# Kernel optimization log

Hardware: AMD Instinct MI355X
Metric: run time of the kernel (lower is better)

Reference implementation:

```python
import jax, jax.numpy as jnp
import numpy as np

B, L, K, NRBF = 2, 2048, 32, 16
NODE_F, EDGE_F = 128, 128
MAX_REL = 32  # af2 relpos -> 2*32+1 = 65 bins
NODE_IN, EDGE_IN = 21 + 6 + 8, 65 + 25 * NRBF + 1 + 2


def _ln(x, g, b, eps=1e-5):
    mu = jnp.mean(x, -1, keepdims=True)
    var = jnp.var(x, -1, keepdims=True)
    return (x - mu) / jnp.sqrt(var + eps) * g + b


def _normalize(t):
    return jnp.nan_to_num(t / jnp.linalg.norm(t, axis=-1, keepdims=True))


def _dihedral(p0, p1, p2, p3):
    u0, u1, u2 = p2 - p1, p0 - p1, p3 - p2
    n1 = _normalize(jnp.cross(u0, u1))
    n2 = _normalize(jnp.cross(u0, u2))
    sgn = jnp.sign(jnp.sum(jnp.cross(u1, u2) * u0, -1))
    return jnp.nan_to_num(sgn * jnp.arccos(jnp.sum(n1 * n2, -1)))


def setup_inputs() -> dict:
    key = jax.random.key(0)
    ks = jax.random.split(key, 9)
    return {
        "X": jax.random.normal(ks[0], (B, L, 4, 3), jnp.float32) * 5.0,
        "S": jax.random.randint(ks[1], (B, L), 0, 21),
        "BB_D_sincos": jax.random.normal(ks[2], (B, L, 3, 2), jnp.float32),
        "SC_D_sincos": jax.random.normal(ks[3], (B, L, 4, 2), jnp.float32),
        "chain_indices": jax.random.randint(ks[4], (B, L), 0, 2),
        "mask": jnp.ones((B, L), jnp.float32),
        "W_node": jax.random.normal(ks[5], (NODE_IN, NODE_F), jnp.float32) * 0.05,
        "b_node": jnp.zeros((NODE_F,), jnp.float32),
        "g_node": jnp.ones((NODE_F,), jnp.float32),
        "beta_node": jnp.zeros((NODE_F,), jnp.float32),
        "W_edge": jax.random.normal(ks[6], (EDGE_IN, EDGE_F), jnp.float32) * 0.05,
        "b_edge": jnp.zeros((EDGE_F,), jnp.float32),
        "g_edge": jnp.ones((EDGE_F,), jnp.float32),
        "beta_edge": jnp.zeros((EDGE_F,), jnp.float32),
    }


def reference(X, S, BB_D_sincos, SC_D_sincos, chain_indices, mask,
              W_node, b_node, g_node, beta_node,
              W_edge, b_edge, g_edge, beta_edge):
    Bn, Ln = X.shape[:2]
    N, Ca, C, O = X[:, :, 0], X[:, :, 1], X[:, :, 2], X[:, :, 3]
    # ---- masked pairwise Ca distances + kNN topk (smallest) ----
    m2 = mask[:, None, :] * mask[:, :, None]                      # [B,L,L]
    dX = Ca[:, :, None, :] - Ca[:, None, :, :]
    D = m2 * jnp.sqrt(jnp.sum(dX * dX, -1) + 1e-6)
    D_adj = D + 2.0 * (1.0 - m2) * jnp.max(D, -1, keepdims=True)
    _, E_idx = jax.lax.top_k(-D_adj, K)                           # [B,L,K]
    bidx = jnp.arange(Bn)[:, None, None]
    # ---- af2 relative-position one-hot (residue_index=None path) ----
    offset = E_idx - jnp.arange(Ln)[None, :, None]
    E_pos = jax.nn.one_hot(jnp.clip(offset + MAX_REL, 0, 2 * MAX_REL),
                           2 * MAX_REL + 1, dtype=jnp.float32)    # [B,L,K,65]
    # ---- impute CB, 5x5 atomic-distance RBFs at neighbors only ----
    bv, cv = Ca - N, C - Ca
    Cb = -0.58273431 * jnp.cross(bv, cv) + 0.56802827 * bv - 0.54067466 * cv + Ca
    X5 = jnp.stack((N, Ca, C, O, Cb), axis=-2)                    # [B,L,5,3]
    X5_nb = X5[bidx, E_idx]                                       # [B,L,K,5,3]
    dA = X5[:, :, None, :, None, :] - X5_nb[:, :, :, None, :, :]  # [B,L,K,5i,5j,3]
    Dn = jnp.sqrt(jnp.sum(dA * dA, -1) + 1e-6)                    # [B,L,K,5,5]
    mu = jnp.linspace(0.0, 20.0, NRBF)
    sigma = 20.0 / NRBF
    RBF_all = jnp.exp(-(((Dn[..., None] - mu) / sigma) ** 2))
    RBF_all = RBF_all.reshape(Bn, Ln, K, 25 * NRBF)               # i-major, j, rbf order
    # ---- edge type: same-chain indicator + 1 ----
    ch_nb = chain_indices[bidx, E_idx]
    E_type = ((ch_nb == chain_indices[:, :, None]).astype(jnp.float32) + 1.0)[..., None]
    # ---- pairwise dihedrals, evaluated only at neighbors ----
    N_nb, Ca_nb, C_nb = N[bidx, E_idx], Ca[bidx, E_idx], C[bidx, E_idx]
    ir_phi = _dihedral(C[:, :, None, :], N_nb, Ca_nb, C_nb)
    ir_psi = _dihedral(N[:, :, None, :], Ca[:, :, None, :], C[:, :, None, :], N_nb)
    dihed = jnp.stack((ir_phi, ir_psi), -1)                       # [B,L,K,2]
    # ---- fuse + embed ----
    E = jnp.concatenate((E_pos, RBF_all, E_type, dihed), -1)      # [B,L,K,468]
    V = jnp.concatenate((jax.nn.one_hot(S, 21, dtype=jnp.float32),
                         BB_D_sincos.reshape(Bn, Ln, -1),
                         SC_D_sincos.reshape(Bn, Ln, -1)), -1)    # [B,L,35]
    h_V = _ln(V @ W_node + b_node, g_node, beta_node)
    h_E = _ln(E @ W_edge + b_edge, g_edge, beta_edge)
    return (h_V, h_E, E_idx, X)
```

## Files before the change

kernel.cpp:

```cpp
#include <hip/hip_runtime.h>
#include <math.h>

#define NB 2
#define NL 2048
#define NK 32
#define NODE_F 128
#define EDGE_F 128

#define OFF_HV   0
#define OFF_HE   (NB*NL*NODE_F)
#define OFF_EIDX (OFF_HE + NB*NL*NK*EDGE_F)
#define OFF_X    (OFF_EIDX + NB*NL*NK)

#define ACH 8
#define BCH 8
#define SAW 264
#define NCH 16

typedef __attribute__((ext_vector_type(8))) short v8s;
typedef __attribute__((ext_vector_type(4))) float v4f;

__device__ __forceinline__ short f2bf(float f) {
    unsigned u = __float_as_uint(f);
    unsigned r = u + 0x7fffu + ((u >> 16) & 1u);
    return (short)(r >> 16);
}

#if __has_builtin(__builtin_amdgcn_exp2f)
#define EXP2F(x) __builtin_amdgcn_exp2f(x)
#else
#define EXP2F(x) __expf((x) * 0.6931471805599453f)
#endif

__device__ __forceinline__ unsigned bfpack(float f0, float f1) {
    unsigned u0 = __float_as_uint(f0), u1 = __float_as_uint(f1);
#if __has_builtin(__builtin_amdgcn_perm)
    return __builtin_amdgcn_perm(u1, u0, 0x07060302u);
#else
    return (u1 & 0xFFFF0000u) | (u0 >> 16);
#endif
}

template<int CTRL>
__device__ __forceinline__ float dpp_add_f32(float x) {
    int p = __builtin_amdgcn_update_dpp(0, __float_as_int(x), CTRL, 0xF, 0xF, true);
    return x + __int_as_float(p);
}
template<int CTRL>
__device__ __forceinline__ float dpp_max_f32(float x) {
    int p = __builtin_amdgcn_update_dpp(0, __float_as_int(x), CTRL, 0xF, 0xF, true);
    return fmaxf(x, __int_as_float(p));
}
__device__ __forceinline__ float dpp_row_sum16(float x) {
    x = dpp_add_f32<0x111>(x);
    x = dpp_add_f32<0x112>(x);
    x = dpp_add_f32<0x114>(x);
    x = dpp_add_f32<0x118>(x);
    return x;
}
__device__ __forceinline__ float dpp_wave_sum(float x) {
    x = dpp_row_sum16(x);
    x = dpp_add_f32<0x142>(x);
    x = dpp_add_f32<0x143>(x);
    return __int_as_float(__builtin_amdgcn_readlane(__float_as_int(x), 63));
}
__device__ __forceinline__ float dpp_wave_max_nn(float x) {
    x = dpp_max_f32<0x111>(x);
    x = dpp_max_f32<0x112>(x);
    x = dpp_max_f32<0x114>(x);
    x = dpp_max_f32<0x118>(x);
    x = dpp_max_f32<0x142>(x);
    x = dpp_max_f32<0x143>(x);
    return __int_as_float(__builtin_amdgcn_readlane(__float_as_int(x), 63));
}

template<int J>
__device__ __forceinline__ unsigned long long lane_xor64(unsigned long long x) {
    if constexpr (J == 32) {
        return __shfl_xor(x, 32, 64);
    } else {
        unsigned lo = (unsigned)x, hi = (unsigned)(x >> 32);
        if constexpr (J == 1 || J == 2) {
            constexpr int ctrl = (J == 1) ? 0xB1 : 0x4E;
            lo = (unsigned)__builtin_amdgcn_update_dpp((int)lo, (int)lo, ctrl, 0xF, 0xF, false);
            hi = (unsigned)__builtin_amdgcn_update_dpp((int)hi, (int)hi, ctrl, 0xF, 0xF, false);
        } else {
            constexpr int off = (J << 10) | 0x1F;
            lo = (unsigned)__builtin_amdgcn_ds_swizzle((int)lo, off);
            hi = (unsigned)__builtin_amdgcn_ds_swizzle((int)hi, off);
        }
        return (((unsigned long long)hi) << 32) | lo;
    }
}

__device__ __forceinline__ void cross3(const float a[3], const float b[3], float c[3]) {
    c[0] = a[1]*b[2] - a[2]*b[1];
    c[1] = a[2]*b[0] - a[0]*b[2];
    c[2] = a[0]*b[1] - a[1]*b[0];
}
__device__ __forceinline__ float dot3(const float a[3], const float b[3]) {
    return a[0]*b[0] + a[1]*b[1] + a[2]*b[2];
}
__device__ float dihedral_f(const float p0[3], const float p1[3],
                            const float p2[3], const float p3[3]) {
    float u0[3], u1[3], u2[3];
    for (int d = 0; d < 3; d++) {
        u0[d] = p2[d] - p1[d];
        u1[d] = p0[d] - p1[d];
        u2[d] = p3[d] - p2[d];
    }
    float n1[3], n2[3], c12[3];
    cross3(u0, u1, n1);
    cross3(u0, u2, n2);
    cross3(u1, u2, c12);
    float l1 = sqrtf(dot3(n1, n1));
    float l2 = sqrtf(dot3(n2, n2));
    float cosang = dot3(n1, n2) / (l1 * l2);
    float s = dot3(c12, u0);
    float sgn = (s > 0.f) ? 1.f : ((s < 0.f) ? -1.f : 0.f);
    float r = sgn * acosf(cosang);
    return isnan(r) ? 0.f : r;
}

__global__ __launch_bounds__(256) void fused_pre_kernel(const float* __restrict__ X,
                                                        const float* __restrict__ mask,
                                                        const int* __restrict__ S,
                                                        const float* __restrict__ BB,
                                                        const float* __restrict__ SC,
                                                        const float* __restrict__ Wn,
                                                        const float* __restrict__ bn,
                                                        const float* __restrict__ gn,
                                                        const float* __restrict__ betan,
                                                        const float* __restrict__ We,
                                                        const float* __restrict__ be,
                                                        float* __restrict__ X5,
                                                        short* __restrict__ WTf,
                                                        int* __restrict__ EidxW,
                                                        float* __restrict__ out) {
    __shared__ float sCa[NL * 3];
    __shared__ unsigned long long sSel[4][64];
    int blk = blockIdx.x;
    int tid = threadIdx.x;

    if (blk >= 1024) {
        if (blk < 1040) {
            int row = (blk - 1024) * 256 + tid;
            float v[12];
#pragma unroll
            for (int t = 0; t < 12; t++) v[t] = X[row * 12 + t];
#pragma unroll
            for (int t = 0; t < 12; t++) out[OFF_X + row * 12 + t] = v[t];
            float bv[3], cv[3], cr[3];
            for (int d = 0; d < 3; d++) { bv[d] = v[3+d] - v[d]; cv[d] = v[6+d] - v[3+d]; }
            cross3(bv, cv, cr);
            float* x5 = X5 + row * 15;
#pragma unroll
            for (int t = 0; t < 12; t++) x5[t] = v[t];
            for (int d = 0; d < 3; d++)
                x5[12 + d] = -0.58273431f * cr[d] + 0.56802827f * bv[d] - 0.54067466f * cv[d] + v[3+d];
        } else {
            int t = (blk - 1040) * 256 + tid;
            if (t >= NCH * 8 * 64) return;
            int lane = t & 63;
            int nt = (t >> 6) & 7;
            int ch = t >> 9;
            int n = nt * 16 + (lane & 15);
            int kbase = ch * 32 + (lane >> 4) * 8;
            short* dst = WTf + (size_t)t * 8;
#pragma unroll
            for (int j = 0; j < 8; j++) {
                int k = kbase + j;
                float f;
                if (k < 403) f = We[(65 + k) * 128 + n];
                else if (k == 403) f = be[n];
                else if (k <= 468) f = We[(k - 404) * 128 + n];
                else f = 0.f;
                dst[j] = f2bf(f);
            }
        }
        return;
    }

    int w = tid >> 6, l = tid & 63;
    int row = blk * 4 + w;
    int b = row / NL;
    int base = b * NL;

    for (int idx = tid; idx < NL; idx += 256) {
        const float* xp = X + (size_t)(base + idx) * 12 + 3;
        sCa[idx * 3 + 0] = xp[0];
        sCa[idx * 3 + 1] = xp[1];
        sCa[idx * 3 + 2] = xp[2];
    }

    {
        int f0 = l, f1 = 64 + l;
        int s = S[row];
        float a0 = bn[f0] + Wn[s * NODE_F + f0];
        float a1 = bn[f1] + Wn[s * NODE_F + f1];
#pragma unroll
        for (int t = 0; t < 6; t++) {
            float x = BB[row * 6 + t];
            a0 += x * Wn[(21 + t) * NODE_F + f0];
            a1 += x * Wn[(21 + t) * NODE_F + f1];
        }
#pragma unroll
        for (int t = 0; t < 8; t++) {
            float x = SC[row * 8 + t];
            a0 += x * Wn[(27 + t) * NODE_F + f0];
            a1 += x * Wn[(27 + t) * NODE_F + f1];
        }
        float tot = dpp_wave_sum(a0 + a1);
        float mean = tot * (1.0f / 128.0f);
        float d0 = a0 - mean, d1 = a1 - mean;
        float qt = dpp_wave_sum(d0 * d0 + d1 * d1);
        float rstd = 1.0f / sqrtf(qt * (1.0f / 128.0f) + 1e-5f);
        out[OFF_HV + row * NODE_F + f0] = d0 * rstd * gn[f0] + betan[f0];
        out[OFF_HV + row * NODE_F + f1] = d1 * rstd * gn[f1] + betan[f1];
    }
    __syncthreads();

    const float* mrow = mask + base;
    int lrow = row - base;
    float cx = sCa[lrow * 3 + 0], cy = sCa[lrow * 3 + 1], cz = sCa[lrow * 3 + 2];
    float mi = mrow[lrow];

    float K[32];
    float lmax = 0.0f;
#pragma unroll
    for (int t = 0; t < 32; t++) {
        int j = t * 64 + l;
        float dx = __fsub_rn(cx, sCa[j * 3 + 0]);
        float dy = __fsub_rn(cy, sCa[j * 3 + 1]);
        float dz = __fsub_rn(cz, sCa[j * 3 + 2]);
        float ss = __fadd_rn(__fadd_rn(__fadd_rn(__fmul_rn(dx, dx), __fmul_rn(dy, dy)),
                                       __fmul_rn(dz, dz)), 1e-6f);
        float d = __fmul_rn(__fmul_rn(mi, mrow[j]), __fsqrt_rn(ss));
        K[t] = d;
        lmax = fmaxf(lmax, d);
    }
    lmax = dpp_wave_max_nn(lmax);
#pragma unroll
    for (int t = 0; t < 32; t++) {
        int j = t * 64 + l;
        float m2 = __fmul_rn(mi, mrow[j]);
        K[t] = __fadd_rn(K[t], __fmul_rn(__fmul_rn(2.0f, __fsub_rn(1.0f, m2)), lmax));
    }

    unsigned lo_ = 0u, hi_ = 0x7f7fffffu, tau = 0x7f7fffffu;
#pragma unroll 1
    for (int it = 0; it < 31; it++) {
        unsigned mid = (lo_ + hi_) >> 1;
        float tf = __uint_as_float(mid);
        int c = 0;
#pragma unroll
        for (int t = 0; t < 32; t++) c += __popcll(__ballot(K[t] <= tf));
        if (c >= 32) {
            tau = mid;
            if (c <= 64) break;
            hi_ = mid - 1;
        } else {
            lo_ = mid + 1;
        }
    }
    float tauf = __uint_as_float(tau);

    sSel[w][l] = ~0ull;
    int cbase = 0;
#pragma unroll
    for (int t = 0; t < 32; t++) {
        bool q = (K[t] <= tauf);
        unsigned long long m = __ballot(q);
        int pos = cbase + __popcll(m & ((1ull << l) - 1ull));
        if (q && pos < 64)
            sSel[w][pos] = (((unsigned long long)__float_as_uint(K[t])) << 32)
                           | (unsigned)(t * 64 + l);
        cbase += __popcll(m);
    }

    unsigned long long key = sSel[w][l];
#define BSTAGE(K_, J_) {                                                       \
    unsigned long long o_ = lane_xor64<J_>(key);                               \
    bool keepMin = (((l & (K_)) == 0) == ((l & (J_)) == 0));                   \
    unsigned long long mn_ = key < o_ ? key : o_;                              \
    key = keepMin ? mn_ : (key ^ o_ ^ mn_);                                    \
}
    BSTAGE(2, 1)
    BSTAGE(4, 2)  BSTAGE(4, 1)
    BSTAGE(8, 4)  BSTAGE(8, 2)  BSTAGE(8, 1)
    BSTAGE(16, 8) BSTAGE(16, 4) BSTAGE(16, 2) BSTAGE(16, 1)
    BSTAGE(32, 16) BSTAGE(32, 8) BSTAGE(32, 4) BSTAGE(32, 2) BSTAGE(32, 1)
    BSTAGE(64, 32) BSTAGE(64, 16) BSTAGE(64, 8) BSTAGE(64, 4) BSTAGE(64, 2) BSTAGE(64, 1)

    if (l < NK) {
        int selj = (int)(unsigned)key;
        EidxW[row * NK + l] = selj;
        out[OFF_EIDX + row * NK + l] = (float)selj;
    }
}

__global__ __launch_bounds__(256, 4) void edge11_kernel(const float* __restrict__ X5,
                                                        const int* __restrict__ Eidx,
                                                        const int* __restrict__ chain,
                                                        const float* __restrict__ ge,
                                                        const float* __restrict__ betae,
                                                        const short* __restrict__ WTf,
                                                        float* __restrict__ out) {
    __shared__ short sA[64 * SAW];
    __shared__ float sXj[64][17];
    __shared__ float sXi[2][15];
    __shared__ int   sJ[64];
    __shared__ int   sPos[64];
    __shared__ float sEt[64], sPhi[64], sPsi[64];

    int tid = threadIdx.x;
    int e0 = blockIdx.x * 64;
    int b = e0 / (NL * NK);
    int i0 = (e0 / NK) % NL;
    int lane = tid & 63, w = tid >> 6;

    if (tid < 64) sJ[tid] = Eidx[e0 + tid];
    if (tid < 30) sXi[tid / 15][tid % 15] = X5[(b * NL + i0 + tid / 15) * 15 + (tid % 15)];
    __syncthreads();

    for (int t = tid; t < 64 * 15; t += 256) {
        int e = t / 15, c2 = t % 15;
        sXj[e][c2] = X5[(b * NL + sJ[e]) * 15 + c2];
    }
    if (tid < 64) {
        int e = tid;
        int i = i0 + (e >> 5);
        int j = sJ[e];
        int off = j - i + 32;
        off = off < 0 ? 0 : (off > 64 ? 64 : off);
        sPos[e] = off;
        sEt[e] = (chain[b * NL + j] == chain[b * NL + i]) ? 2.0f : 1.0f;
    }
    __syncthreads();

    if (tid < 128) {
        int e = tid & 63;
        const float* xi = sXi[e >> 5];
        const float* xj = sXj[e];
        if (tid < 64) sPhi[e] = dihedral_f(&xi[6], &xj[0], &xj[3], &xj[6]);
        else          sPsi[e] = dihedral_f(&xi[0], &xi[3], &xi[6], &xj[0]);
    }

    const float Ac  = -0.92332482616893658f;
    const float K1c = 2.46219953645049755f;
    const float Rc  = EXP2F(-1.64146635763366503f);
    const float R2c = Rc * Rc;
    int eg_ = w * 16 + (lane & 15);
    int q_ = lane >> 4;
    const float* xiG = sXi[eg_ >> 5];
    const float* xjG = sXj[eg_];
    short* rowp = sA + eg_ * SAW;
    int posG = sPos[eg_];

#define SPECV(k) ((k) == 400 ? sEt[eg_] : (k) == 401 ? sPhi[eg_] : (k) == 402 ? sPsi[eg_] : \
                  (k) == 403 ? 1.0f : (((k) - 404 == posG) ? 1.0f : 0.0f))

#define GEN_A(hh)                                                              \
    {                                                                          \
        _Pragma("unroll")                                                      \
        for (int t = 0; t < 4; t++) {                                          \
            int pl = q_ + t * 4;                         \
            int p  = (hh) * 16 + pl;                          \
            union { unsigned u[8]; v8s v[2]; } au;                             \
            if ((hh) == 1 && p >= 25) {                                        \
                _Pragma("unroll")                                              \
                for (int jp = 0; jp < 8; jp++) {                               \
                    int k0 = p * 16 + 2 * jp;                                  \
                    au.u[jp] = bfpack(SPECV(k0), SPECV(k0 + 1));               \
                }                                                              \
            } else {                                                           \
                int a = p / 5, cc = p - a * 5;                                 \
                float dx = xiG[a*3+0] - xjG[cc*3+0];                           \
                float dy = xiG[a*3+1] - xjG[cc*3+1];                           \
                float dz = xiG[a*3+2] - xjG[cc*3+2];                           \
                float d = sqrtf(dx*dx + dy*dy + dz*dz + 1e-6f);                \
                float ee = fminf(d, 40.f);                                     \
                float r0 = EXP2F(Ac * ee * ee);                                \
                float g  = EXP2F(K1c * ee) * Rc;                               \
                float r1  = r0  * g; g *= R2c;                                 \
                float r2  = r1  * g; g *= R2c;                                 \
                float r3  = r2  * g; g *= R2c;                                 \
                float r4  = r3  * g; g *= R2c;                                 \
                float r5  = r4  * g; g *= R2c;                                 \
                float r6  = r5  * g; g *= R2c;                                 \
                float r7  = r6  * g; g *= R2c;                                 \
                float r8  = r7  * g; g *= R2c;                                 \
                float r9  = r8  * g; g *= R2c;                                 \
                float r10 = r9  * g; g *= R2c;                                 \
                float r11 = r10 * g; g *= R2c;                                 \
                float r12 = r11 * g; g *= R2c;                                 \
                float r13 = r12 * g; g *= R2c;                                 \
                float r14 = r13 * g; g *= R2c;                                 \
                float r15 = r14 * g;                                           \
                au.u[0] = bfpack(r0,  r1);                                     \
                au.u[1] = bfpack(r2,  r3);                                     \
                au.u[2] = bfpack(r4,  r5);                                     \
                au.u[3] = bfpack(r6,  r7);                                     \
                au.u[4] = bfpack(r8,  r9);                                     \
                au.u[5] = bfpack(r10, r11);                                    \
                au.u[6] = bfpack(r12, r13);                                    \
                au.u[7] = bfpack(r14, r15);                                    \
            }                                                                  \
            *(v8s*)(rowp + pl * 16)     = au.v[0];                             \
            *(v8s*)(rowp + pl * 16 + 8) = au.v[1];                             \
        }                                                                      \
    }

    GEN_A(0)
    __syncthreads();

    int cl = lane & 15, kq = lane >> 4;
    int ntA = 2 * w, ntB = ntA + 1;
    const char* sAc = (const char*)sA;
    int abase0 = cl * (SAW * 2) + kq * 16;

    v4f acc[4][2];
#pragma unroll
    for (int eg = 0; eg < 4; eg++) { acc[eg][0] = (v4f){0.f,0.f,0.f,0.f}; acc[eg][1] = (v4f){0.f,0.f,0.f,0.f}; }

#define MMA_HALF(CHBASE, CNT)                                                  \
    {                                                                          \
        _Pragma("unroll 2")                                                    \
        for (int chl = 0; chl < (CNT); chl++) {                                \
            const v8s* gb = (const v8s*)WTf + ((size_t)((CHBASE) + chl) * 512 + lane); \
            v8s b0 = gb[ntA * 64];                                             \
            v8s b1 = gb[ntB * 64];                                             \
            int ab = abase0 + chl * 64;                                        \
            v8s a0 = *(const v8s*)(sAc + ab);                                  \
            v8s a1 = *(const v8s*)(sAc + ab + 16 * (SAW * 2));                 \
            v8s a2 = *(const v8s*)(sAc + ab + 32 * (SAW * 2));                 \
            v8s a3 = *(const v8s*)(sAc + ab + 48 * (SAW * 2));                 \
            acc[0][0] = __builtin_amdgcn_mfma_f32_16x16x32_bf16(a0, b0, acc[0][0], 0, 0, 0); \
            acc[0][1] = __builtin_amdgcn_mfma_f32_16x16x32_bf16(a0, b1, acc[0][1], 0, 0, 0); \
            acc[1][0] = __builtin_amdgcn_mfma_f32_16x16x32_bf16(a1, b0, acc[1][0], 0, 0, 0); \
            acc[1][1] = __builtin_amdgcn_mfma_f32_16x16x32_bf16(a1, b1, acc[1][1], 0, 0, 0); \
            acc[2][0] = __builtin_amdgcn_mfma_f32_16x16x32_bf16(a2, b0, acc[2][0], 0, 0, 0); \
            acc[2][1] = __builtin_amdgcn_mfma_f32_16x16x32_bf16(a2, b1, acc[2][1], 0, 0, 0); \
            acc[3][0] = __builtin_amdgcn_mfma_f32_16x16x32_bf16(a3, b0, acc[3][0], 0, 0, 0); \
            acc[3][1] = __builtin_amdgcn_mfma_f32_16x16x32_bf16(a3, b1, acc[3][1], 0, 0, 0); \
        }                                                                      \
    }

    MMA_HALF(0, ACH)
    __syncthreads();
    GEN_A(1)
    __syncthreads();
    MMA_HALF(ACH, BCH)

    float2* sRed = (float2*)&sXj[0][0];
    int nA = ntA * 16 + cl, nB = nA + 16;
    float r4A = ge[nA], r5A = betae[nA];
    float r4B = ge[nB], r5B = betae[nB];

#pragma unroll
    for (int eg = 0; eg < 4; eg++) {
#pragma unroll
        for (int r = 0; r < 4; r++) {
            int e = eg * 16 + kq * 4 + r;
            float v0 = acc[eg][0][r];
            float v1 = acc[eg][1][r];
            float s  = dpp_row_sum16(v0 + v1);
            float q2 = dpp_row_sum16(v0 * v0 + v1 * v1);
            if (cl == 15) sRed[e * 4 + w] = make_float2(s, q2);
        }
    }
    __syncthreads();

#pragma unroll
    for (int eg = 0; eg < 4; eg++) {
#pragma unroll
        for (int r = 0; r < 4; r++) {
            int e = eg * 16 + kq * 4 + r;
            float4 pa = *(const float4*)&sRed[e * 4];
            float4 pb = *(const float4*)&sRed[e * 4 + 2];
            float s  = pa.x + pa.z + pb.x + pb.z;
            float q2 = pa.y + pa.w + pb.y + pb.w;
            float mean = s * (1.0f / 128.0f);
            float var = q2 * (1.0f / 128.0f) - mean * mean;
            float rstd = rsqrtf(var + 1e-5f);
            size_t base = OFF_HE + (size_t)(e0 + e) * 128;
            out[base + nA] = (acc[eg][0][r] - mean) * rstd * r4A + r5A;
            out[base + nB] = (acc[eg][1][r] - mean) * rstd * r4B + r5B;
        }
    }
}

extern "C" void kernel_launch(void* const* d_in, const int* in_sizes, int n_in,
                              void* d_out, int out_size, void* d_ws, size_t ws_size,
                              hipStream_t stream) {
    (void)in_sizes; (void)n_in; (void)out_size; (void)ws_size;
    const float* X    = (const float*)d_in[0];
    const int*   S    = (const int*)d_in[1];
    const float* BB   = (const float*)d_in[2];
    const float* SC   = (const float*)d_in[3];
    const int*   chain= (const int*)d_in[4];
    const float* mask = (const float*)d_in[5];
    const float* Wn   = (const float*)d_in[6];
    const float* bn   = (const float*)d_in[7];
    const float* gn   = (const float*)d_in[8];
    const float* betan= (const float*)d_in[9];
    const float* We   = (const float*)d_in[10];
    const float* be   = (const float*)d_in[11];
    const float* ge   = (const float*)d_in[12];
    const float* betae= (const float*)d_in[13];
    float* out = (float*)d_out;

    char* ws = (char*)d_ws;
    int*   EidxW = (int*)ws;
    float* X5    = (float*)(ws + 524288);
    short* WTf   = (short*)(ws + 770048);

    hipLaunchKernelGGL(fused_pre_kernel, dim3(1024 + 16 + 32), dim3(256), 0, stream,
                       X, mask, S, BB, SC, Wn, bn, gn, betan, We, be,
                       X5, WTf, EidxW, out);
    hipLaunchKernelGGL(edge11_kernel, dim3(NB * NL * NK / 64), dim3(256), 0, stream,
                       X5, EidxW, chain, ge, betae, WTf, out);
}
```

Measured before the change: 152.2 us.

## Split edge A-tile generation into quarters to shrink LDS and raise occupancy

The edge kernel now builds its bf16 feature tile in four quarter-width chunks of 128 columns instead of two halves of 256. Each chunk is followed by an MFMA pass, which roughly halves the shared-memory A buffer (64x136 shorts). That allows launch bounds of 6 blocks per CU instead of 4. In exchange the kernel gains extra __syncthreads barriers and lower per-block ILP between generation and matmul, and the register budget is tighter under the higher occupancy target.

```diff
diff --git a/kernel.cpp b/kernel.cpp
--- a/kernel.cpp
+++ b/kernel.cpp
@@ -12,10 +12,8 @@
 #define OFF_EIDX (OFF_HE + NB*NL*NK*EDGE_F)
 #define OFF_X    (OFF_EIDX + NB*NL*NK)
 
-#define ACH 8
-#define BCH 8
-#define SAW 264
 #define NCH 16
+#define SAWQ 136
 
 typedef __attribute__((ext_vector_type(8))) short v8s;
 typedef __attribute__((ext_vector_type(4))) float v4f;
@@ -299,14 +297,14 @@
     }
 }
 
-__global__ __launch_bounds__(256, 4) void edge11_kernel(const float* __restrict__ X5,
+__global__ __launch_bounds__(256, 6) void edge12_kernel(const float* __restrict__ X5,
                                                         const int* __restrict__ Eidx,
                                                         const int* __restrict__ chain,
                                                         const float* __restrict__ ge,
                                                         const float* __restrict__ betae,
                                                         const short* __restrict__ WTf,
                                                         float* __restrict__ out) {
-    __shared__ short sA[64 * SAW];
+    __shared__ short sA[64 * SAWQ];
     __shared__ float sXj[64][17];
     __shared__ float sXi[2][15];
     __shared__ int   sJ[64];
@@ -354,20 +352,20 @@
     int q_ = lane >> 4;
     const float* xiG = sXi[eg_ >> 5];
     const float* xjG = sXj[eg_];
-    short* rowp = sA + eg_ * SAW;
+    short* rowp = sA + eg_ * SAWQ;
     int posG = sPos[eg_];
 
 #define SPECV(k) ((k) == 400 ? sEt[eg_] : (k) == 401 ? sPhi[eg_] : (k) == 402 ? sPsi[eg_] : \
                   (k) == 403 ? 1.0f : (((k) - 404 == posG) ? 1.0f : 0.0f))
 
-#define GEN_A(hh)                                                              \
+#define GEN_A(qq)                                                              \
     {                                                                          \
         _Pragma("unroll")                                                      \
-        for (int t = 0; t < 4; t++) {                                          \
-            int pl = q_ + t * 4;                         \
-            int p  = (hh) * 16 + pl;                          \
+        for (int t = 0; t < 2; t++) {                                          \
+            int pl = q_ + t * 4;                          \
+            int p  = (qq) * 8 + pl;                           \
             union { unsigned u[8]; v8s v[2]; } au;                             \
-            if ((hh) == 1 && p >= 25) {                                        \
+            if ((qq) == 3 && p >= 25) {                                        \
                 _Pragma("unroll")                                              \
                 for (int jp = 0; jp < 8; jp++) {                               \
                     int k0 = p * 16 + 2 * jp;                                  \
@@ -411,30 +409,27 @@
         }                                                                      \
     }
 
-    GEN_A(0)
-    __syncthreads();
-
     int cl = lane & 15, kq = lane >> 4;
     int ntA = 2 * w, ntB = ntA + 1;
     const char* sAc = (const char*)sA;
-    int abase0 = cl * (SAW * 2) + kq * 16;
+    int abase0 = cl * (SAWQ * 2) + kq * 16;
 
     v4f acc[4][2];
 #pragma unroll
     for (int eg = 0; eg < 4; eg++) { acc[eg][0] = (v4f){0.f,0.f,0.f,0.f}; acc[eg][1] = (v4f){0.f,0.f,0.f,0.f}; }
 
-#define MMA_HALF(CHBASE, CNT)                                                  \
+#define MMA_Q(QQ)                                                              \
     {                                                                          \
-        _Pragma("unroll 2")                                                    \
-        for (int chl = 0; chl < (CNT); chl++) {                                \
-            const v8s* gb = (const v8s*)WTf + ((size_t)((CHBASE) + chl) * 512 + lane); \
+        _Pragma("unroll")                                                      \
+        for (int chl = 0; chl < 4; chl++) {                                    \
+            const v8s* gb = (const v8s*)WTf + ((size_t)((QQ) * 4 + chl) * 512 + lane); \
             v8s b0 = gb[ntA * 64];                                             \
             v8s b1 = gb[ntB * 64];                                             \
             int ab = abase0 + chl * 64;                                        \
             v8s a0 = *(const v8s*)(sAc + ab);                                  \
-            v8s a1 = *(const v8s*)(sAc + ab + 16 * (SAW * 2));                 \
-            v8s a2 = *(const v8s*)(sAc + ab + 32 * (SAW * 2));                 \
-            v8s a3 = *(const v8s*)(sAc + ab + 48 * (SAW * 2));                 \
+            v8s a1 = *(const v8s*)(sAc + ab + 16 * (SAWQ * 2));                \
+            v8s a2 = *(const v8s*)(sAc + ab + 32 * (SAWQ * 2));                \
+            v8s a3 = *(const v8s*)(sAc + ab + 48 * (SAWQ * 2));                \
             acc[0][0] = __builtin_amdgcn_mfma_f32_16x16x32_bf16(a0, b0, acc[0][0], 0, 0, 0); \
             acc[0][1] = __builtin_amdgcn_mfma_f32_16x16x32_bf16(a0, b1, acc[0][1], 0, 0, 0); \
             acc[1][0] = __builtin_amdgcn_mfma_f32_16x16x32_bf16(a1, b0, acc[1][0], 0, 0, 0); \
@@ -446,11 +441,21 @@
         }                                                                      \
     }
 
-    MMA_HALF(0, ACH)
+    GEN_A(0)
+    __syncthreads();
+    MMA_Q(0)
     __syncthreads();
     GEN_A(1)
     __syncthreads();
-    MMA_HALF(ACH, BCH)
+    MMA_Q(1)
+    __syncthreads();
+    GEN_A(2)
+    __syncthreads();
+    MMA_Q(2)
+    __syncthreads();
+    GEN_A(3)
+    __syncthreads();
+    MMA_Q(3)
 
     float2* sRed = (float2*)&sXj[0][0];
     int nA = ntA * 16 + cl, nB = nA + 16;
@@ -518,6 +523,6 @@
     hipLaunchKernelGGL(fused_pre_kernel, dim3(1024 + 16 + 32), dim3(256), 0, stream,
                        X, mask, S, BB, SC, Wn, bn, gn, betan, We, be,
                        X5, WTf, EidxW, out);
-    hipLaunchKernelGGL(edge11_kernel, dim3(NB * NL * NK / 64), dim3(256), 0, stream,
+    hipLaunchKernelGGL(edge12_kernel, dim3(NB * NL * NK / 64), dim3(256), 0, stream,
                        X5, EidxW, chain, ge, betae, WTf, out);
 }
```

Measured after the change: 161.4 us. +6.1%, slower.
